# Performance work log

Measured on AMD Instinct MI355X. Metric: run time of the kernel, lower is better.

## Reference

```python
import jax, jax.numpy as jnp
import numpy as np

B, C, H, W = 16, 256, 56, 56
G, K, R = 16, 3, 2
CR = C // R          # reduced channels = 128
KKG = K * K * G      # span output channels = 144
EPS = 1e-5


def setup_inputs() -> dict:
    key = jax.random.key(0)
    ks = jax.random.split(key, 5)
    return {
        "x": jax.random.normal(ks[0], (B, C, H, W), jnp.float32),
        "w_reduce": jax.random.normal(ks[1], (CR, C), jnp.float32) * 0.05,
        "b_reduce": jax.random.normal(ks[2], (CR,), jnp.float32) * 0.05,
        "gamma": jnp.ones((CR,), jnp.float32),
        "beta": jnp.zeros((CR,), jnp.float32),
        "w_span": jax.random.normal(ks[3], (KKG, CR), jnp.float32) * 0.05,
        "b_span": jax.random.normal(ks[4], (KKG,), jnp.float32) * 0.05,
    }


def _conv1x1(x, w, bias):
    # 1x1 conv == channel contraction
    return jnp.einsum('bchw,oc->bohw', x, w) + bias[None, :, None, None]


def _involution(x, w_reduce, b_reduce, gamma, beta, w_span, b_span):
    b, c, h, w = x.shape
    # kernel-generation branch: reduce -> BN (batch stats) -> ReLU -> span
    t = _conv1x1(x, w_reduce, b_reduce)
    mu = t.mean(axis=(0, 2, 3), keepdims=True)
    var = t.var(axis=(0, 2, 3), keepdims=True)  # biased, as torch BN training
    t = (t - mu) * jax.lax.rsqrt(var + EPS)
    t = t * gamma[None, :, None, None] + beta[None, :, None, None]
    t = jax.nn.relu(t)
    kern = _conv1x1(t, w_span, b_span)  # [b, k*k*g, h, w]
    # 'b (k j g) h w -> b g (k j) h w'
    kern = kern.reshape(b, K, K, G, h, w).transpose(0, 3, 1, 2, 4, 5)
    kern = kern.reshape(b, G, K * K, h, w)
    # unfold x into [b, g, d, k*k, h, w] via shifted padded slices (no dense im2col buffer write pattern beyond necessity)
    p = K // 2
    xp = jnp.pad(x, ((0, 0), (0, 0), (p, p), (p, p)))
    patches = jnp.stack(
        [xp[:, :, i:i + h, j:j + w] for i in range(K) for j in range(K)],
        axis=2)  # [b, c, k*k, h, w]
    patches = patches.reshape(b, G, c // G, K * K, h, w)
    out = jnp.einsum('bgdxhw,bgxhw->bgdhw', patches, kern)  # weighted window sum
    return out.reshape(b, c, h, w)


def reference(x, w_reduce, b_reduce, gamma, beta, w_span, b_span):
    return _involution(x, w_reduce, b_reduce, gamma, beta, w_span, b_span)
```

## Files before the change

kernel.cpp:

```cpp
#include <hip/hip_runtime.h>
#include <hip/hip_bf16.h>

#define B_   16
#define C_   256
#define HW_  3136
#define W_   56
#define CR_  128
#define KKG_ 144
#define G_   16
#define NPOS (B_*HW_)
#define EPS_ 1e-5f
#define NBLK1 1568
#define NBLK3 784

typedef float f32x4 __attribute__((ext_vector_type(4)));
typedef short s16x8 __attribute__((ext_vector_type(8)));

#define T2_OFF_B    0
#define KERN_OFF_B  12845056
#define GP_OFF_B    27295744
#define STAT_OFF_B  28901376
#define WBFR_OFF_B  28902400
#define WBFS_OFF_B  28967936

__device__ inline unsigned short f2bf(float f) {
    unsigned u = __float_as_uint(f);
    u += 0x7fff + ((u >> 16) & 1);
    return (unsigned short)(u >> 16);
}
__device__ inline float bf2f(unsigned short h) {
    return __uint_as_float(((unsigned)h) << 16);
}
__device__ inline unsigned pkcvt(float a, float b) {
    float2 f2; f2.x = a; f2.y = b;
    __hip_bfloat162 h = __float22bfloat162_rn(f2);
    union { __hip_bfloat162 h2; unsigned u; } cv; cv.h2 = h;
    return cv.u;
}

typedef const __attribute__((address_space(1))) unsigned int* gas_t;
typedef __attribute__((address_space(3))) unsigned int* las_t;
__device__ inline void gload_lds16(const void* g, void* l) {
    __builtin_amdgcn_global_load_lds((gas_t)g, (las_t)l, 16, 0, 0);
}
__device__ inline void barrier_raw() {
    __builtin_amdgcn_sched_barrier(0);
    __builtin_amdgcn_s_barrier();
    __builtin_amdgcn_sched_barrier(0);
}

__global__ __launch_bounds__(256) void prep_cast(
    const float* __restrict__ w_reduce, const float* __restrict__ w_span,
    unsigned short* __restrict__ wbfr, unsigned short* __restrict__ wbfs)
{
    int idx = blockIdx.x * 256 + threadIdx.x;
    if (idx < 32768) {
        wbfr[idx] = f2bf(w_reduce[idx]);
    } else {
        int k = idx - 32768;
        if (k < 18432) wbfs[k] = f2bf(w_span[k]);
    }
}

__global__ __launch_bounds__(256, 4) void reduce_mfma(
    const float* __restrict__ x, const unsigned short* __restrict__ wbfr,
    unsigned short* __restrict__ t2, float* __restrict__ gp)
{
    __shared__ __align__(16) float xb3[3][1024];
    __shared__ __align__(16) short awb[3][4096];
    __shared__ float redp[128][2], redq[128][2];

    const int tid = threadIdx.x;
    const int lane = tid & 63, wv = tid >> 6;
    const int q = lane >> 4, i = lane & 15;
    const int q8 = q * 8;
    const int mrow = (wv & 1) * 64;
    const int pw = (wv >> 1) * 16;
    const int blk = blockIdx.x;
    const int b = blk / 98;
    const int p0 = (blk % 98) * 32;

    const int c_st = tid >> 3;
    const int swz = ((tid & 7) ^ ((c_st >> 1) & 7)) * 4;
    const float* xlane = x + (size_t)b * C_ * HW_ + (size_t)c_st * HW_ + p0 + swz;
    const unsigned short* wA0 = wbfr + (size_t)(tid >> 2) * C_ + (tid & 3) * 8;
    const unsigned short* wA1 = wA0 + (size_t)64 * C_;
    float* xdst_base = (float*)0;
    const int wvu4 = (tid & ~63) * 4;
    const int wvu8 = (tid & ~63) * 8;

    #define STAGE1(ch, bi) do {                                          \
        gload_lds16(xlane + (size_t)(ch) * 32 * HW_, &xb3[bi][wvu4]);    \
        gload_lds16(wA0 + (ch) * 32, &awb[bi][wvu8]);                    \
        gload_lds16(wA1 + (ch) * 32, &awb[bi][2048 + wvu8]);             \
    } while (0)

    const int p_loc = pw + i;
    const int pg = p_loc >> 2, pe = p_loc & 3;

    f32x4 acc[4] = {};

    STAGE1(0, 0);
    STAGE1(1, 1);

    #pragma unroll
    for (int ch = 0; ch < 8; ch++) {
        const int cur = ch % 3;
        if (ch < 7) asm volatile("s_waitcnt vmcnt(3)" ::: "memory");
        else        asm volatile("s_waitcnt vmcnt(0)" ::: "memory");
        barrier_raw();
        if (ch == 0) STAGE1(2, 2);
        if (ch == 1) STAGE1(3, 0);
        if (ch == 2) STAGE1(4, 1);
        if (ch == 3) STAGE1(5, 2);
        if (ch == 4) STAGE1(6, 0);
        if (ch == 5) STAGE1(7, 1);

        s16x8 af[4];
        #pragma unroll
        for (int mt = 0; mt < 4; mt++)
            af[mt] = *(const s16x8*)&awb[cur][(mrow + mt * 16 + i) * 32 + q8];
        float f[8];
        #pragma unroll
        for (int k = 0; k < 8; k++) {
            int cl = q8 + k;
            int slot = pg ^ ((cl >> 1) & 7);
            f[k] = xb3[cur][cl * 32 + slot * 4 + pe];
        }
        union { s16x8 v; unsigned u[4]; } Bv;
        #pragma unroll
        for (int k2 = 0; k2 < 4; k2++) Bv.u[k2] = pkcvt(f[2*k2], f[2*k2+1]);

        #pragma unroll
        for (int mt = 0; mt < 4; mt++)
            acc[mt] = __builtin_amdgcn_mfma_f32_16x16x32_bf16(
                af[mt], Bv.v, acc[mt], 0, 0, 0);
    }
    #undef STAGE1

    const int p = p0 + pw + i;
    #pragma unroll
    for (int mt = 0; mt < 4; mt++) {
        uint2 pr;
        pr.x = pkcvt(acc[mt][0], acc[mt][1]);
        pr.y = pkcvt(acc[mt][2], acc[mt][3]);
        *(uint2*)(t2 + ((size_t)b * HW_ + p) * CR_ + mrow + mt * 16 + q * 4) = pr;
        #pragma unroll
        for (int reg = 0; reg < 4; reg++) {
            float v = acc[mt][reg];
            float s = v, ss = v * v;
            #pragma unroll
            for (int m = 1; m < 16; m <<= 1) {
                s  += __shfl_xor(s, m);
                ss += __shfl_xor(ss, m);
            }
            if (i == 0) {
                int o = mrow + mt * 16 + q * 4 + reg;
                redp[o][wv >> 1] = s;
                redq[o][wv >> 1] = ss;
            }
        }
    }
    __syncthreads();
    if (tid < 128)
        gp[(size_t)tid * NBLK1 + blk] = redp[tid][0] + redp[tid][1];
    else
        gp[(size_t)tid * NBLK1 + blk] = redq[tid - 128][0] + redq[tid - 128][1];
}

__global__ __launch_bounds__(256) void bn_finalize(
    const float* __restrict__ gp, const float* __restrict__ gamma,
    const float* __restrict__ beta, float* __restrict__ stats)
{
    const int o = blockIdx.x;
    const int tid = threadIdx.x;
    float s = 0.f, ss = 0.f;
    for (int idx = tid; idx < NBLK1; idx += 256) {
        s  += gp[(size_t)o * NBLK1 + idx];
        ss += gp[(size_t)(128 + o) * NBLK1 + idx];
    }
    #pragma unroll
    for (int m = 1; m < 64; m <<= 1) {
        s  += __shfl_xor(s, m);
        ss += __shfl_xor(ss, m);
    }
    __shared__ float rs[4], rss[4];
    if ((tid & 63) == 0) { rs[tid >> 6] = s; rss[tid >> 6] = ss; }
    __syncthreads();
    if (tid == 0) {
        s  = rs[0] + rs[1] + rs[2] + rs[3];
        ss = rss[0] + rss[1] + rss[2] + rss[3];
        float inv_n = 1.0f / (float)NPOS;
        float mu = s * inv_n;
        float var = ss * inv_n - mu * mu;
        float sc = gamma[o] * rsqrtf(var + EPS_);
        stats[o] = sc;
        stats[128 + o] = beta[o] - mu * sc;
    }
}

__global__ __launch_bounds__(256, 3) void span_mfma(
    const unsigned short* __restrict__ t2, const unsigned short* __restrict__ wbfs,
    const float* __restrict__ b_span, const float* __restrict__ stats,
    unsigned short* __restrict__ kern)
{
    __shared__ __align__(16) short aw[144 * 128];
    __shared__ __align__(16) short bb3[3][2048];
    __shared__ float scs[128], shs[128], bsp[144];

    const int tid = threadIdx.x;
    const int lane = tid & 63, wv = tid >> 6;
    const int q = lane >> 4, i = lane & 15;
    const int q8 = q * 8;
    const int blk = blockIdx.x;
    const int b = blk / 49;
    const int p0 = (blk % 49) * 64;

    if (tid < 128) { scs[tid] = stats[tid]; shs[tid] = stats[128 + tid]; }
    if (tid < 144) bsp[tid] = b_span[tid];
    __syncthreads();

    const unsigned short* tlane =
        t2 + ((size_t)b * HW_ + p0 + (tid >> 2)) * CR_ + (tid & 3) * 8;
    const int wvu8 = (tid & ~63) * 8;

    #pragma unroll
    for (int e = 0; e < 9; e++) {
        int U = tid + e * 256;
        int r = U >> 4, u = U & 15;
        gload_lds16(wbfs + (size_t)r * CR_ + ((u ^ (r & 7)) * 8),
                    &aw[((tid & ~63) + e * 256) * 8]);
    }
    gload_lds16(tlane,      &bb3[0][wvu8]);
    gload_lds16(tlane + 32, &bb3[1][wvu8]);

    f32x4 acc[9] = {};

    #pragma unroll
    for (int ch = 0; ch < 4; ch++) {
        const int cur = ch % 3;
        if (ch < 3) asm volatile("s_waitcnt vmcnt(1)" ::: "memory");
        else        asm volatile("s_waitcnt vmcnt(0)" ::: "memory");
        barrier_raw();
        if (ch == 0) gload_lds16(tlane + 64, &bb3[2][wvu8]);
        if (ch == 1) gload_lds16(tlane + 96, &bb3[0][wvu8]);

        s16x8 raw = *(const s16x8*)&bb3[cur][(wv * 16 + i) * 32 + q8];
        const int cb = ch * 32 + q8;
        float f[8];
        #pragma unroll
        for (int k = 0; k < 8; k++)
            f[k] = fmaxf(fmaf(bf2f((unsigned short)raw[k]),
                              scs[cb + k], shs[cb + k]), 0.0f);
        union { s16x8 v; unsigned u[4]; } Bv;
        #pragma unroll
        for (int k2 = 0; k2 < 4; k2++) Bv.u[k2] = pkcvt(f[2*k2], f[2*k2+1]);

        #pragma unroll
        for (int mt = 0; mt < 9; mt++) {
            int r = mt * 16 + i;
            int slot = (ch * 4 + q) ^ (r & 7);
            s16x8 af = *(const s16x8*)&aw[r * 128 + slot * 8];
            acc[mt] = __builtin_amdgcn_mfma_f32_16x16x32_bf16(
                af, Bv.v, acc[mt], 0, 0, 0);
        }
    }

    const int p = p0 + wv * 16 + i;
    #pragma unroll
    for (int mt = 0; mt < 9; mt++) {
        #pragma unroll
        for (int reg = 0; reg < 4; reg++) {
            int o2 = mt * 16 + q * 4 + reg;
            int row = (o2 & 15) * 9 + (o2 >> 4);
            kern[((size_t)b * KKG_ + row) * HW_ + p] = f2bf(acc[mt][reg] + bsp[o2]);
        }
    }
}

__global__ __launch_bounds__(256) void involution_apply(
    const float* __restrict__ x, const unsigned short* __restrict__ kern,
    float* __restrict__ out)
{
    int gtid = blockIdx.x * 256 + threadIdx.x;
    int pix = gtid % HW_;
    int bg  = gtid / HW_;
    int g = bg & 15;
    int b = bg >> 4;
    int h = pix / W_;
    int w = pix % W_;

    const unsigned short* kb = kern + ((size_t)(b * G_ + g) * 9) * HW_ + pix;
    float kv[9];
    #pragma unroll
    for (int kk = 0; kk < 9; kk++)
        kv[kk] = bf2f(kb[(size_t)kk * HW_]);

    float acc[16];
    #pragma unroll
    for (int d = 0; d < 16; d++) acc[d] = 0.0f;

    const float* xb = x + (size_t)(b * C_ + g * 16) * HW_;
    #pragma unroll
    for (int di = 0; di < 3; di++) {
        int hh = h + di - 1;
        if (hh < 0 || hh >= W_) continue;
        #pragma unroll
        for (int dj = 0; dj < 3; dj++) {
            int ww = w + dj - 1;
            if (ww < 0 || ww >= W_) continue;
            float kval = kv[di * 3 + dj];
            int off = hh * W_ + ww;
            #pragma unroll
            for (int d = 0; d < 16; d++)
                acc[d] = fmaf(xb[(size_t)d * HW_ + off], kval, acc[d]);
        }
    }
    float* ob = out + (size_t)(b * C_ + g * 16) * HW_ + pix;
    #pragma unroll
    for (int d = 0; d < 16; d++) ob[(size_t)d * HW_] = acc[d];
}

extern "C" void kernel_launch(void* const* d_in, const int* in_sizes, int n_in,
                              void* d_out, int out_size, void* d_ws, size_t ws_size,
                              hipStream_t stream) {
    const float* x        = (const float*)d_in[0];
    const float* w_reduce = (const float*)d_in[1];
    const float* gamma    = (const float*)d_in[3];
    const float* beta     = (const float*)d_in[4];
    const float* w_span   = (const float*)d_in[5];
    const float* b_span   = (const float*)d_in[6];
    float* out = (float*)d_out;

    char* wsb = (char*)d_ws;
    unsigned short* t2   = (unsigned short*)(wsb + T2_OFF_B);
    unsigned short* kern = (unsigned short*)(wsb + KERN_OFF_B);
    float*          gp    = (float*)(wsb + GP_OFF_B);
    float*          stats = (float*)(wsb + STAT_OFF_B);
    unsigned short* wbfr = (unsigned short*)(wsb + WBFR_OFF_B);
    unsigned short* wbfs = (unsigned short*)(wsb + WBFS_OFF_B);

    prep_cast<<<200, 256, 0, stream>>>(w_reduce, w_span, wbfr, wbfs);
    reduce_mfma<<<NBLK1, 256, 0, stream>>>(x, wbfr, t2, gp);
    bn_finalize<<<128, 256, 0, stream>>>(gp, gamma, beta, stats);
    span_mfma<<<NBLK3, 256, 0, stream>>>(t2, wbfs, b_span, stats, kern);
    involution_apply<<<(B_ * G_ * HW_) / 256, 256, 0, stream>>>(x, kern, out);
}
```

Measured before the change: 170.7 us.

## Fold BN finalize into atomics and span prologue; vectorize involution apply over 4 pixels

Removes the bn_finalize kernel. Each reduce block now atomically adds its per-channel sum and sum-of-squares into a 256-float accumulator, zeroed in prep_cast, and span_mfma computes scale and shift from it in its prologue. Separately, involution_apply now has each thread handle 4 consecutive pixels for all 16 channels of a group, using float4 loads for x and the output plus vectorized bf16 kernel loads, so shared halo values are reused across neighbouring pixels. The trade-offs are atomic contention (1568 blocks on 256 addresses), a non-deterministic summation order, and more registers per thread in the apply kernel.

```diff
diff --git a/kernel.cpp b/kernel.cpp
--- a/kernel.cpp
+++ b/kernel.cpp
@@ -15,13 +15,13 @@
 
 typedef float f32x4 __attribute__((ext_vector_type(4)));
 typedef short s16x8 __attribute__((ext_vector_type(8)));
+typedef short s16x4 __attribute__((ext_vector_type(4)));
 
 #define T2_OFF_B    0
 #define KERN_OFF_B  12845056
-#define GP_OFF_B    27295744
-#define STAT_OFF_B  28901376
-#define WBFR_OFF_B  28902400
-#define WBFS_OFF_B  28967936
+#define GACC_OFF_B  27295744
+#define WBFR_OFF_B  27296768
+#define WBFS_OFF_B  27362304
 
 __device__ inline unsigned short f2bf(float f) {
     unsigned u = __float_as_uint(f);
@@ -51,9 +51,11 @@
 
 __global__ __launch_bounds__(256) void prep_cast(
     const float* __restrict__ w_reduce, const float* __restrict__ w_span,
-    unsigned short* __restrict__ wbfr, unsigned short* __restrict__ wbfs)
+    unsigned short* __restrict__ wbfr, unsigned short* __restrict__ wbfs,
+    float* __restrict__ gacc)
 {
     int idx = blockIdx.x * 256 + threadIdx.x;
+    if (idx < 256) gacc[idx] = 0.0f;
     if (idx < 32768) {
         wbfr[idx] = f2bf(w_reduce[idx]);
     } else {
@@ -64,7 +66,7 @@
 
 __global__ __launch_bounds__(256, 4) void reduce_mfma(
     const float* __restrict__ x, const unsigned short* __restrict__ wbfr,
-    unsigned short* __restrict__ t2, float* __restrict__ gp)
+    unsigned short* __restrict__ t2, float* __restrict__ gacc)
 {
     __shared__ __align__(16) float xb3[3][1024];
     __shared__ __align__(16) short awb[3][4096];
@@ -85,7 +87,6 @@
     const float* xlane = x + (size_t)b * C_ * HW_ + (size_t)c_st * HW_ + p0 + swz;
     const unsigned short* wA0 = wbfr + (size_t)(tid >> 2) * C_ + (tid & 3) * 8;
     const unsigned short* wA1 = wA0 + (size_t)64 * C_;
-    float* xdst_base = (float*)0;
     const int wvu4 = (tid & ~63) * 4;
     const int wvu8 = (tid & ~63) * 8;
 
@@ -162,46 +163,14 @@
         }
     }
     __syncthreads();
-    if (tid < 128)
-        gp[(size_t)tid * NBLK1 + blk] = redp[tid][0] + redp[tid][1];
-    else
-        gp[(size_t)tid * NBLK1 + blk] = redq[tid - 128][0] + redq[tid - 128][1];
-}
-
-__global__ __launch_bounds__(256) void bn_finalize(
-    const float* __restrict__ gp, const float* __restrict__ gamma,
-    const float* __restrict__ beta, float* __restrict__ stats)
-{
-    const int o = blockIdx.x;
-    const int tid = threadIdx.x;
-    float s = 0.f, ss = 0.f;
-    for (int idx = tid; idx < NBLK1; idx += 256) {
-        s  += gp[(size_t)o * NBLK1 + idx];
-        ss += gp[(size_t)(128 + o) * NBLK1 + idx];
-    }
-    #pragma unroll
-    for (int m = 1; m < 64; m <<= 1) {
-        s  += __shfl_xor(s, m);
-        ss += __shfl_xor(ss, m);
-    }
-    __shared__ float rs[4], rss[4];
-    if ((tid & 63) == 0) { rs[tid >> 6] = s; rss[tid >> 6] = ss; }
-    __syncthreads();
-    if (tid == 0) {
-        s  = rs[0] + rs[1] + rs[2] + rs[3];
-        ss = rss[0] + rss[1] + rss[2] + rss[3];
-        float inv_n = 1.0f / (float)NPOS;
-        float mu = s * inv_n;
-        float var = ss * inv_n - mu * mu;
-        float sc = gamma[o] * rsqrtf(var + EPS_);
-        stats[o] = sc;
-        stats[128 + o] = beta[o] - mu * sc;
-    }
+    if (tid < 128) atomicAdd(&gacc[tid], redp[tid][0] + redp[tid][1]);
+    else           atomicAdd(&gacc[tid], redq[tid - 128][0] + redq[tid - 128][1]);
 }
 
 __global__ __launch_bounds__(256, 3) void span_mfma(
     const unsigned short* __restrict__ t2, const unsigned short* __restrict__ wbfs,
-    const float* __restrict__ b_span, const float* __restrict__ stats,
+    const float* __restrict__ b_span, const float* __restrict__ gacc,
+    const float* __restrict__ gamma, const float* __restrict__ beta,
     unsigned short* __restrict__ kern)
 {
     __shared__ __align__(16) short aw[144 * 128];
@@ -216,7 +185,15 @@
     const int b = blk / 49;
     const int p0 = (blk % 49) * 64;
 
-    if (tid < 128) { scs[tid] = stats[tid]; shs[tid] = stats[128 + tid]; }
+    if (tid < 128) {
+        float s = gacc[tid], ss = gacc[128 + tid];
+        const float inv_n = 1.0f / (float)NPOS;
+        float mu = s * inv_n;
+        float var = ss * inv_n - mu * mu;
+        float sc = gamma[tid] * rsqrtf(var + EPS_);
+        scs[tid] = sc;
+        shs[tid] = beta[tid] - mu * sc;
+    }
     if (tid < 144) bsp[tid] = b_span[tid];
     __syncthreads();
 
@@ -282,43 +259,58 @@
     const float* __restrict__ x, const unsigned short* __restrict__ kern,
     float* __restrict__ out)
 {
-    int gtid = blockIdx.x * 256 + threadIdx.x;
-    int pix = gtid % HW_;
-    int bg  = gtid / HW_;
-    int g = bg & 15;
-    int b = bg >> 4;
-    int h = pix / W_;
-    int w = pix % W_;
-
-    const unsigned short* kb = kern + ((size_t)(b * G_ + g) * 9) * HW_ + pix;
-    float kv[9];
-    #pragma unroll
-    for (int kk = 0; kk < 9; kk++)
-        kv[kk] = bf2f(kb[(size_t)kk * HW_]);
-
-    float acc[16];
-    #pragma unroll
-    for (int d = 0; d < 16; d++) acc[d] = 0.0f;
-
-    const float* xb = x + (size_t)(b * C_ + g * 16) * HW_;
-    #pragma unroll
-    for (int di = 0; di < 3; di++) {
-        int hh = h + di - 1;
-        if (hh < 0 || hh >= W_) continue;
-        #pragma unroll
-        for (int dj = 0; dj < 3; dj++) {
-            int ww = w + dj - 1;
-            if (ww < 0 || ww >= W_) continue;
-            float kval = kv[di * 3 + dj];
-            int off = hh * W_ + ww;
+    const int gtid = blockIdx.x * 256 + threadIdx.x;
+    const int pu  = gtid % 784;
+    const int bg  = gtid / 784;
+    const int g = bg & 15;
+    const int b = bg >> 4;
+    const int pix0 = pu * 4;
+    const int h = pix0 / W_;
+    const int w0 = pix0 % W_;
+
+    const unsigned short* kb = kern + ((size_t)(b * G_ + g) * 9) * HW_ + pix0;
+    float kvf[9][4];
+    #pragma unroll
+    for (int kk = 0; kk < 9; kk++) {
+        s16x4 kraw = *(const s16x4*)(kb + (size_t)kk * HW_);
+        #pragma unroll
+        for (int j = 0; j < 4; j++)
+            kvf[kk][j] = bf2f((unsigned short)kraw[j]);
+    }
+
+    const float* xg = x + (size_t)(b * C_ + g * 16) * HW_;
+    float* og = out + (size_t)(b * C_ + g * 16) * HW_ + pix0;
+
+    const bool has_l = (w0 > 0);
+    const bool has_r = (w0 + 4 < W_);
+    const int loff = has_l ? (w0 - 1) : w0;
+    const int roff = has_r ? (w0 + 4) : w0;
+
+    #pragma unroll
+    for (int d = 0; d < 16; d++) {
+        f32x4 acc = {0.0f, 0.0f, 0.0f, 0.0f};
+        const float* xd = xg + (size_t)d * HW_;
+        #pragma unroll
+        for (int di = 0; di < 3; di++) {
+            const int hh = h + di - 1;
+            if (hh < 0 || hh >= W_) continue;
+            const float* xr = xd + hh * W_;
+            float4 mid = *(const float4*)(xr + w0);
+            float lv = xr[loff];
+            float rv = xr[roff];
+            float win[6];
+            win[0] = has_l ? lv : 0.0f;
+            win[1] = mid.x; win[2] = mid.y; win[3] = mid.z; win[4] = mid.w;
+            win[5] = has_r ? rv : 0.0f;
             #pragma unroll
-            for (int d = 0; d < 16; d++)
-                acc[d] = fmaf(xb[(size_t)d * HW_ + off], kval, acc[d]);
-        }
-    }
-    float* ob = out + (size_t)(b * C_ + g * 16) * HW_ + pix;
-    #pragma unroll
-    for (int d = 0; d < 16; d++) ob[(size_t)d * HW_] = acc[d];
+            for (int dj = 0; dj < 3; dj++) {
+                #pragma unroll
+                for (int j = 0; j < 4; j++)
+                    acc[j] = fmaf(win[dj + j], kvf[di * 3 + dj][j], acc[j]);
+            }
+        }
+        *(f32x4*)(og + (size_t)d * HW_) = acc;
+    }
 }
 
 extern "C" void kernel_launch(void* const* d_in, const int* in_sizes, int n_in,
@@ -335,14 +327,12 @@
     char* wsb = (char*)d_ws;
     unsigned short* t2   = (unsigned short*)(wsb + T2_OFF_B);
     unsigned short* kern = (unsigned short*)(wsb + KERN_OFF_B);
-    float*          gp    = (float*)(wsb + GP_OFF_B);
-    float*          stats = (float*)(wsb + STAT_OFF_B);
+    float*          gacc = (float*)(wsb + GACC_OFF_B);
     unsigned short* wbfr = (unsigned short*)(wsb + WBFR_OFF_B);
     unsigned short* wbfs = (unsigned short*)(wsb + WBFS_OFF_B);
 
-    prep_cast<<<200, 256, 0, stream>>>(w_reduce, w_span, wbfr, wbfs);
-    reduce_mfma<<<NBLK1, 256, 0, stream>>>(x, wbfr, t2, gp);
-    bn_finalize<<<128, 256, 0, stream>>>(gp, gamma, beta, stats);
-    span_mfma<<<NBLK3, 256, 0, stream>>>(t2, wbfs, b_span, stats, kern);
-    involution_apply<<<(B_ * G_ * HW_) / 256, 256, 0, stream>>>(x, kern, out);
-}
+    prep_cast<<<200, 256, 0, stream>>>(w_reduce, w_span, wbfr, wbfs, gacc);
+    reduce_mfma<<<NBLK1, 256, 0, stream>>>(x, wbfr, t2, gacc);
+    span_mfma<<<NBLK3, 256, 0, stream>>>(t2, wbfs, b_span, gacc, gamma, beta, kern);
+    involution_apply<<<(B_ * G_ * HW_ / 4) / 256, 256, 0, stream>>>(x, kern, out);
+}
```

Measured after the change: 198.8 us. +16.5%, slower.
